# Kernel optimization log

Measured on AMD Instinct MI355X. Metric: run time of the kernel, lower is better.

## Reference

```python
import jax, jax.numpy as jnp
import numpy as np

N_NODES = 100000
FEAT = 128
EMBED = 128
BATCH = 4096
NUM_SAMPLE = 10


def setup_inputs() -> dict:
    key = jax.random.key(0)
    k1, k2, k3, k4 = jax.random.split(key, 4)
    features = jax.random.normal(k1, (N_NODES, FEAT), dtype=jnp.float32)
    # per-node weight, xavier-uniform-like scale
    lim = np.sqrt(6.0 / (2 * FEAT + EMBED)).astype(np.float32)
    weight = jax.random.uniform(k2, (BATCH, 2 * FEAT, EMBED), dtype=jnp.float32, minval=-lim, maxval=lim)
    nodes = jax.random.randint(k3, (BATCH,), 0, N_NODES, dtype=jnp.int64 if jax.config.jax_enable_x64 else jnp.int32)
    neigh_idx = jax.random.randint(k4, (BATCH, NUM_SAMPLE), 0, N_NODES, dtype=nodes.dtype)
    return {"features": features, "weight": weight, "nodes": nodes, "neigh_idx": neigh_idx}


def reference(features, weight, nodes, neigh_idx):
    # MeanAggregator: gather sampled neighbor features and average -> [B, F]
    neigh_feats = features[neigh_idx].mean(axis=1)
    # self embedding lookup -> [B, F]
    self_feats = features[nodes]
    # concat -> [B, 2F]
    combined = jnp.concatenate([self_feats, neigh_feats], axis=1)
    # per-node batched matmul: [B,1,2F] x [B,2F,E] -> [B,E], then ReLU
    out = jax.nn.relu(jnp.einsum("bi,bie->be", combined, weight))
    return out
```

## Files before the change

kernel.cpp:

```cpp
#include <hip/hip_runtime.h>


constexpr int FEAT  = 128;
constexpr int EMBED = 128;
constexpr int NSAMP = 10;
constexpr int TWOF  = 2 * FEAT;

typedef float v4f __attribute__((ext_vector_type(4)));

__global__ __launch_bounds__(256) void encoder_kernel(
    const float* __restrict__ features,
    const float* __restrict__ weight,
    const int*   __restrict__ nodes,
    const int*   __restrict__ neigh_idx,
    float*       __restrict__ out)
{
    const int b = blockIdx.x;
    const int t = threadIdx.x;

    __shared__ float c[TWOF];
    __shared__ float partial[8 * 128];

    float gval;
    if (t < FEAT) {
        const int node = nodes[b];
        gval = features[(size_t)node * FEAT + t];
    } else {
        const int f = t - FEAT;
        float s = 0.f;
#pragma unroll
        for (int k = 0; k < NSAMP; ++k) {
            const int n = neigh_idx[b * NSAMP + k];
            s += features[(size_t)n * FEAT + f];
        }
        gval = s * (1.0f / NSAMP);
    }

    const int quad = t & 31;
    const int seg  = t >> 5;
    const v4f* __restrict__ wtile =
        (const v4f*)(weight + (size_t)b * TWOF * EMBED)
        + (size_t)seg * 32 * 32 + quad;

    v4f w[8];
#pragma unroll
    for (int j = 0; j < 8; ++j)
        w[j] = __builtin_nontemporal_load(wtile + j * 32);

    c[t] = gval;
    __syncthreads();

    float accx = 0.f, accy = 0.f, accz = 0.f, accw = 0.f;
#pragma unroll
    for (int chunk = 0; chunk < 4; ++chunk) {
        v4f wn[8];
        if (chunk < 3) {
#pragma unroll
            for (int j = 0; j < 8; ++j)
                wn[j] = __builtin_nontemporal_load(wtile + ((chunk + 1) * 8 + j) * 32);
        }
#pragma unroll
        for (int j = 0; j < 8; ++j) {
            const float ci = c[seg * 32 + chunk * 8 + j];
            accx = fmaf(ci, w[j].x, accx);
            accy = fmaf(ci, w[j].y, accy);
            accz = fmaf(ci, w[j].z, accz);
            accw = fmaf(ci, w[j].w, accw);
        }
        if (chunk < 3) {
#pragma unroll
            for (int j = 0; j < 8; ++j) w[j] = wn[j];
        }
    }

    float* p = &partial[seg * 128 + quad * 4];
    p[0] = accx; p[1] = accy; p[2] = accz; p[3] = accw;
    __syncthreads();

    if (t < EMBED) {
        float s = 0.f;
#pragma unroll
        for (int sgi = 0; sgi < 8; ++sgi)
            s += partial[sgi * 128 + t];
        out[(size_t)b * EMBED + t] = fmaxf(s, 0.f);
    }
}

extern "C" void kernel_launch(void* const* d_in, const int* in_sizes, int n_in,
                              void* d_out, int out_size, void* d_ws, size_t ws_size,
                              hipStream_t stream) {
    const float* features = (const float*)d_in[0];
    const float* weight   = (const float*)d_in[1];
    const int*   nodes    = (const int*)d_in[2];
    const int*   neigh    = (const int*)d_in[3];
    float*       outp     = (float*)d_out;

    const int batch = in_sizes[2];
    encoder_kernel<<<batch, 256, 0, stream>>>(features, weight, nodes, neigh, outp);
}
```

Before: 676.1 us.

## Process four batch rows per block with cross-row weight and gather prefetch

Each block now handles four consecutive batch rows. While computing the current row it prefetches the next row's first weight chunk and gathers that row's features into a double-buffered shared array. This hides per-row startup latency from the gather and the first weight loads. In exchange the grid is four times smaller, register use rises, and occupancy may drop.

Result: no change. 685.6 us (+1.4%).

```diff
diff --git a/kernel.cpp b/kernel.cpp
--- a/kernel.cpp
+++ b/kernel.cpp
@@ -5,6 +5,8 @@
 constexpr int EMBED = 128;
 constexpr int NSAMP = 10;
 constexpr int TWOF  = 2 * FEAT;
+constexpr int BPB   = 4;
+constexpr int WV4   = TWOF * EMBED / 4;
 
 typedef float v4f __attribute__((ext_vector_type(4)));
 
@@ -13,76 +15,127 @@
     const float* __restrict__ weight,
     const int*   __restrict__ nodes,
     const int*   __restrict__ neigh_idx,
-    float*       __restrict__ out)
+    float*       __restrict__ out,
+    const int    batch)
 {
-    const int b = blockIdx.x;
-    const int t = threadIdx.x;
+    const int t    = threadIdx.x;
+    const int quad = t & 31;
+    const int seg  = t >> 5;
+    const int b0   = blockIdx.x * BPB;
+    if (b0 >= batch) return;
 
-    __shared__ float c[TWOF];
+    __shared__ float c[2][TWOF];
     __shared__ float partial[8 * 128];
 
-    float gval;
+    int nd[BPB];
+    int ni[BPB][NSAMP];
+#pragma unroll
+    for (int i = 0; i < BPB; ++i) {
+        const int bb = (b0 + i < batch) ? (b0 + i) : (batch - 1);
+        nd[i] = nodes[bb];
+#pragma unroll
+        for (int k = 0; k < NSAMP; ++k) ni[i][k] = neigh_idx[bb * NSAMP + k];
+    }
+
+    const int f = t - FEAT;
+
+    float g;
     if (t < FEAT) {
-        const int node = nodes[b];
-        gval = features[(size_t)node * FEAT + t];
+        g = features[(size_t)nd[0] * FEAT + t];
     } else {
-        const int f = t - FEAT;
         float s = 0.f;
 #pragma unroll
-        for (int k = 0; k < NSAMP; ++k) {
-            const int n = neigh_idx[b * NSAMP + k];
-            s += features[(size_t)n * FEAT + f];
-        }
-        gval = s * (1.0f / NSAMP);
+        for (int k = 0; k < NSAMP; ++k)
+            s += features[(size_t)ni[0][k] * FEAT + f];
+        g = s * (1.0f / NSAMP);
     }
 
-    const int quad = t & 31;
-    const int seg  = t >> 5;
-    const v4f* __restrict__ wtile =
-        (const v4f*)(weight + (size_t)b * TWOF * EMBED)
-        + (size_t)seg * 32 * 32 + quad;
+    const v4f* wp = (const v4f*)weight + (size_t)b0 * WV4
+                  + (size_t)seg * 32 * 32 + quad;
 
     v4f w[8];
 #pragma unroll
     for (int j = 0; j < 8; ++j)
-        w[j] = __builtin_nontemporal_load(wtile + j * 32);
+        w[j] = __builtin_nontemporal_load(wp + j * 32);
 
-    c[t] = gval;
+    int buf = 0;
+    c[buf][t] = g;
     __syncthreads();
 
-    float accx = 0.f, accy = 0.f, accz = 0.f, accw = 0.f;
+    for (int i = 0; i < BPB; ++i) {
+        const int b = b0 + i;
+        if (b >= batch) break;
+        const bool haveNext = (i + 1 < BPB) && (b + 1 < batch);
+
+        float accx = 0.f, accy = 0.f, accz = 0.f, accw = 0.f;
+        float rself;
+        float r[NSAMP];
+
 #pragma unroll
-    for (int chunk = 0; chunk < 4; ++chunk) {
-        v4f wn[8];
-        if (chunk < 3) {
+        for (int chunk = 0; chunk < 4; ++chunk) {
+            const bool pf = (chunk < 3) || haveNext;
+            const v4f* src = (chunk < 3) ? (wp + (chunk + 1) * 8 * 32)
+                                         : (wp + WV4);
+            v4f wn[8];
+            if (pf) {
 #pragma unroll
-            for (int j = 0; j < 8; ++j)
-                wn[j] = __builtin_nontemporal_load(wtile + ((chunk + 1) * 8 + j) * 32);
+                for (int j = 0; j < 8; ++j)
+                    wn[j] = __builtin_nontemporal_load(src + j * 32);
+            }
+
+            if (chunk == 0 && haveNext) {
+                if (t < FEAT) {
+                    rself = features[(size_t)nd[i + 1] * FEAT + t];
+                } else {
+#pragma unroll
+                    for (int k = 0; k < NSAMP; ++k)
+                        r[k] = features[(size_t)ni[i + 1][k] * FEAT + f];
+                }
+            }
+
+            const int base = seg * 32 + chunk * 8;
+#pragma unroll
+            for (int j = 0; j < 8; ++j) {
+                const float ci = c[buf][base + j];
+                accx = fmaf(ci, w[j].x, accx);
+                accy = fmaf(ci, w[j].y, accy);
+                accz = fmaf(ci, w[j].z, accz);
+                accw = fmaf(ci, w[j].w, accw);
+            }
+            if (pf) {
+#pragma unroll
+                for (int j = 0; j < 8; ++j) w[j] = wn[j];
+            }
         }
+
+        float* p = &partial[seg * 128 + quad * 4];
+        p[0] = accx; p[1] = accy; p[2] = accz; p[3] = accw;
+
+        if (haveNext) {
+            float gnext;
+            if (t < FEAT) {
+                gnext = rself;
+            } else {
+                float s = 0.f;
 #pragma unroll
-        for (int j = 0; j < 8; ++j) {
-            const float ci = c[seg * 32 + chunk * 8 + j];
-            accx = fmaf(ci, w[j].x, accx);
-            accy = fmaf(ci, w[j].y, accy);
-            accz = fmaf(ci, w[j].z, accz);
-            accw = fmaf(ci, w[j].w, accw);
+                for (int k = 0; k < NSAMP; ++k) s += r[k];
+                gnext = s * (1.0f / NSAMP);
+            }
+            c[buf ^ 1][t] = gnext;
         }
-        if (chunk < 3) {
+        __syncthreads();
+
+        if (t < EMBED) {
+            float s = 0.f;
 #pragma unroll
-            for (int j = 0; j < 8; ++j) w[j] = wn[j];
+            for (int sgi = 0; sgi < 8; ++sgi)
+                s += partial[sgi * 128 + t];
+            out[(size_t)b * EMBED + t] = fmaxf(s, 0.f);
         }
-    }
 
-    float* p = &partial[seg * 128 + quad * 4];
-    p[0] = accx; p[1] = accy; p[2] = accz; p[3] = accw;
-    __syncthreads();
-
-    if (t < EMBED) {
-        float s = 0.f;
-#pragma unroll
-        for (int sgi = 0; sgi < 8; ++sgi)
-            s += partial[sgi * 128 + t];
-        out[(size_t)b * EMBED + t] = fmaxf(s, 0.f);
+        buf ^= 1;
+        wp += WV4;
+        __syncthreads();
     }
 }
 
@@ -96,5 +149,6 @@
     float*       outp     = (float*)d_out;
 
     const int batch = in_sizes[2];
-    encoder_kernel<<<batch, 256, 0, stream>>>(features, weight, nodes, neigh, outp);
+    const int grid  = (batch + BPB - 1) / BPB;
+    encoder_kernel<<<grid, 256, 0, stream>>>(features, weight, nodes, neigh, outp, batch);
 }
```
